# Kernel tuning notes

Measured on AMD Instinct MI355X. Metric: run time of the kernel, lower is better.

Reference implementation:

```python
import jax, jax.numpy as jnp
import numpy as np

G = 8
NEIGHBORS = 9
BN_EPS = 1e-5


def grid_sample_border(feat, grid):
    """Bilinear grid_sample, padding_mode='border', align_corners=False.
    feat: [B,C,H,W], grid: [B,Ho,Wo,2] in [-1,1] -> [B,C,Ho,Wo]."""
    B, C, H, W = feat.shape
    Ho, Wo = grid.shape[1], grid.shape[2]
    gx, gy = grid[..., 0], grid[..., 1]
    ix = jnp.clip(((gx + 1.0) * W - 1.0) * 0.5, 0.0, W - 1.0)
    iy = jnp.clip(((gy + 1.0) * H - 1.0) * 0.5, 0.0, H - 1.0)
    x0 = jnp.floor(ix)
    y0 = jnp.floor(iy)
    wx = (ix - x0).reshape(B, 1, Ho * Wo)
    wy = (iy - y0).reshape(B, 1, Ho * Wo)
    x0i = jnp.clip(x0.astype(jnp.int32), 0, W - 1)
    x1i = jnp.clip(x0i + 1, 0, W - 1)
    y0i = jnp.clip(y0.astype(jnp.int32), 0, H - 1)
    y1i = jnp.clip(y0i + 1, 0, H - 1)
    featf = feat.reshape(B, C, H * W)

    def gather(yi, xi):
        idx = (yi * W + xi).reshape(B, 1, Ho * Wo)
        return jnp.take_along_axis(featf, idx, axis=2)  # [B,C,Ho*Wo]

    v00 = gather(y0i, x0i)
    v01 = gather(y0i, x1i)
    v10 = gather(y1i, x0i)
    v11 = gather(y1i, x1i)
    out = (v00 * (1 - wx) * (1 - wy) + v01 * wx * (1 - wy)
           + v10 * (1 - wx) * wy + v11 * wx * wy)
    return out.reshape(B, C, Ho, Wo)


def bn3d(x, g, b, m, v):
    # inference-mode BatchNorm3d over channel axis 1 of [B,C,N,H,W]
    sh = (1, -1, 1, 1, 1)
    return g.reshape(sh) * (x - m.reshape(sh)) * jax.lax.rsqrt(v.reshape(sh) + BN_EPS) + b.reshape(sh)


def setup_inputs() -> dict:
    key = jax.random.key(0)
    ks = jax.random.split(key, 16)
    B, C, H, W = 2, 64, 256, 320
    ref_feature = jax.random.normal(ks[0], (B, C, H, W), dtype=jnp.float32)
    grid = jax.random.uniform(ks[1], (B, NEIGHBORS * H, W, 2), dtype=jnp.float32, minval=-1.0, maxval=1.0)
    p = lambda k, sh: 0.1 * jax.random.normal(k, sh, dtype=jnp.float32)
    return {
        "ref_feature": ref_feature,
        "grid": grid,
        "conv0_w": p(ks[2], (16, G)),
        "bn0_g": jnp.ones((16,), jnp.float32),
        "bn0_b": jnp.zeros((16,), jnp.float32),
        "bn0_m": p(ks[3], (16,)),
        "bn0_v": jax.random.uniform(ks[4], (16,), jnp.float32, 0.5, 1.5),
        "conv1_w": p(ks[5], (8, 16)),
        "bn1_g": jnp.ones((8,), jnp.float32),
        "bn1_b": jnp.zeros((8,), jnp.float32),
        "bn1_m": p(ks[6], (8,)),
        "bn1_v": jax.random.uniform(ks[7], (8,), jnp.float32, 0.5, 1.5),
        "sim_w": p(ks[8], (1, 8)),
        "sim_b": jnp.zeros((1,), jnp.float32),
    }


def reference(ref_feature, grid, conv0_w, bn0_g, bn0_b, bn0_m, bn0_v,
              conv1_w, bn1_g, bn1_b, bn1_m, bn1_v, sim_w, sim_b):
    B, C, H, W = ref_feature.shape
    Cg = C // G
    x = grid_sample_border(ref_feature, grid)            # [B,C,NB*H,W]
    x = x.reshape(B, G, Cg, NEIGHBORS, H, W)
    ref = ref_feature.reshape(B, G, Cg, H, W)
    corr = jnp.mean(x * ref[:, :, :, None], axis=2)      # [B,G,NB,H,W]
    h = jax.nn.relu(bn3d(jnp.einsum('oc,bcnhw->bonhw', conv0_w, corr), bn0_g, bn0_b, bn0_m, bn0_v))
    h = jax.nn.relu(bn3d(jnp.einsum('oc,bcnhw->bonhw', conv1_w, h), bn1_g, bn1_b, bn1_m, bn1_v))
    s = jnp.einsum('oc,bcnhw->bonhw', sim_w, h) + sim_b.reshape(1, 1, 1, 1, 1)
    return jax.nn.sigmoid(s[:, 0])                        # [B,NB,H,W]
```

## Files before the change

kernel.cpp:

```cpp
#include <hip/hip_runtime.h>
#include <hip/hip_bf16.h>

#define BB  2
#define CC  64
#define HH  256
#define WW  320
#define NNB 9
#define PIX_PER_B (NNB * HH * WW)
#define HW (HH * WW)

typedef unsigned int uint;

#define FEATT_BYTES ((size_t)BB * HH * WW * 64 * sizeof(ushort))
#define NWTS 304

#define OW0 0
#define OB0 128
#define OW1 144
#define OB1 272
#define OSW 280
#define OSB 288

__global__ __launch_bounds__(64) void fw_fold(
    const float* __restrict__ conv0_w, const float* __restrict__ bn0_g,
    const float* __restrict__ bn0_b, const float* __restrict__ bn0_m,
    const float* __restrict__ bn0_v, const float* __restrict__ conv1_w,
    const float* __restrict__ bn1_g, const float* __restrict__ bn1_b,
    const float* __restrict__ bn1_m, const float* __restrict__ bn1_v,
    const float* __restrict__ sim_w, const float* __restrict__ sim_b,
    float* __restrict__ wts) {
  const int t = threadIdx.x;
  if (t < 16) {
    float a = bn0_g[t] * rsqrtf(bn0_v[t] + 1e-5f);
    wts[OB0 + t] = bn0_b[t] - bn0_m[t] * a;
#pragma unroll
    for (int g = 0; g < 8; ++g) wts[OW0 + t * 8 + g] = conv0_w[t * 8 + g] * a;
  } else if (t < 24) {
    int o = t - 16;
    float a = bn1_g[o] * rsqrtf(bn1_v[o] + 1e-5f);
    wts[OB1 + o] = bn1_b[o] - bn1_m[o] * a;
#pragma unroll
    for (int c = 0; c < 16; ++c) wts[OW1 + o * 16 + c] = conv1_w[o * 16 + c] * a;
  } else if (t < 32) {
    wts[OSW + t - 24] = sim_w[t - 24];
    if (t == 31) wts[OSB] = sim_b[0];
  }
}

__global__ __launch_bounds__(256) void fw_transpose(const float* __restrict__ feat,
                                                    ushort* __restrict__ featT) {
  __shared__ float tile[64][65];
  const int b = blockIdx.z, h = blockIdx.y, w0 = blockIdx.x * 64;
  const int tid = threadIdx.x;
#pragma unroll
  for (int it = 0; it < 16; ++it) {
    int idx = it * 256 + tid;
    int c = idx >> 6, w = idx & 63;
    tile[c][w] = feat[((b * CC + c) * HH + h) * WW + w0 + w];
  }
  __syncthreads();
#pragma unroll
  for (int it = 0; it < 16; ++it) {
    int idx = it * 256 + tid;
    int w = idx >> 6, c = idx & 63;
    __hip_bfloat16 v = __float2bfloat16(tile[c][w]);
    featT[((b * HH + h) * WW + w0 + w) * 64 + c] = *(ushort*)&v;
  }
}

__device__ __forceinline__ float blo(uint u) { return __uint_as_float(u << 16); }
__device__ __forceinline__ float bhi(uint u) { return __uint_as_float(u & 0xffff0000u); }

__global__ __launch_bounds__(256) void fw_main4(
    const ushort* __restrict__ featT, const float* __restrict__ grid,
    const float* __restrict__ wts, float* __restrict__ out) {
  const int blk = blockIdx.x;
  const int xcd = blk & 7;
  const int jb = blk >> 3;
  const int b = xcd >> 2;
  const int lblk = jb * 4 + (xcd & 3);

  const int tid = threadIdx.x;
  const int lane = tid & 63;
  const int wid = tid >> 6;
  const int team = lane >> 3;
  const int lj = lane & 7;
  const int wbase = lblk * 256 + wid * 64;

  const ushort* __restrict__ fbT = featT + (size_t)b * ((size_t)HW * 64);

  float wx, wy;
  int off00, offc;
  {
    const int pix = wbase + lane;
    const float2 g2 =
        *(const float2*)(grid + (size_t)2 * ((size_t)b * PIX_PER_B + pix));
    float ix = fminf(fmaxf(((g2.x + 1.0f) * (float)WW - 1.0f) * 0.5f, 0.0f),
                     (float)(WW - 1));
    float iy = fminf(fmaxf(((g2.y + 1.0f) * (float)HH - 1.0f) * 0.5f, 0.0f),
                     (float)(HH - 1));
    int x0 = min((int)floorf(ix), WW - 2);
    int y0 = min((int)floorf(iy), HH - 2);
    wx = ix - (float)x0;
    wy = iy - (float)y0;
    off00 = (y0 * WW + x0) * 64;
    offc = (pix % HW) * 64;
  }

  float pc[8];

#define PERM(S, PX, PY, PO, PQ)                                                \
  {                                                                            \
    int src = (S)*8 + team;                                                    \
    PX = __shfl(wx, src);                                                      \
    PY = __shfl(wy, src);                                                      \
    PO = __shfl(off00, src);                                                   \
    PQ = __shfl(offc, src);                                                    \
  }

#define LOADS(PO, PQ, L)                                                       \
  {                                                                            \
    const ushort* base = fbT + PO + lj * 8;                                    \
    L[0] = *(const uint4*)(base);                                     \
    L[1] = *(const uint4*)(base + 64);                                \
    L[2] = *(const uint4*)(base + WW * 64);                           \
    L[3] = *(const uint4*)(base + WW * 64 + 64);                      \
    L[4] = *(const uint4*)(fbT + PQ + lj * 8);                     \
  }

#define CORRS(S, PX, PY, L)                                                    \
  {                                                                            \
    float e00 = (1.0f - PX) * (1.0f - PY);                                     \
    float e01 = PX * (1.0f - PY);                                              \
    float e10 = (1.0f - PX) * PY;                                              \
    float e11 = PX * PY;                                                       \
    const uint* ua = (const uint*)&L[0];                                       \
    const uint* ub = (const uint*)&L[1];                                       \
    const uint* uc = (const uint*)&L[2];                                       \
    const uint* ud = (const uint*)&L[3];                                       \
    const uint* ur = (const uint*)&L[4];                                       \
    float acc = 0.0f;                                                          \
    _Pragma("unroll") for (int k = 0; k < 4; ++k) {                            \
      float s0 = e00 * blo(ua[k]) + e01 * blo(ub[k]) + e10 * blo(uc[k]) +      \
                 e11 * blo(ud[k]);                                             \
      acc += s0 * blo(ur[k]);                                                  \
      float s1 = e00 * bhi(ua[k]) + e01 * bhi(ub[k]) + e10 * bhi(uc[k]) +      \
                 e11 * bhi(ud[k]);                                             \
      acc += s1 * bhi(ur[k]);                                                  \
    }                                                                          \
    pc[S] = acc * 0.125f;                                                      \
  }

  float px0, py0, px1, py1, px2, py2, px3, py3;
  int po0, pq0, po1, pq1, po2, pq2, po3, pq3;
  uint4 L0[5], L1[5], L2[5], L3[5];

  PERM(0, px0, py0, po0, pq0) LOADS(po0, pq0, L0)
  PERM(1, px1, py1, po1, pq1) LOADS(po1, pq1, L1)
  PERM(2, px2, py2, po2, pq2) LOADS(po2, pq2, L2)
  PERM(3, px3, py3, po3, pq3) LOADS(po3, pq3, L3)
  __builtin_amdgcn_sched_barrier(0);

  CORRS(0, px0, py0, L0)
  PERM(4, px0, py0, po0, pq0) LOADS(po0, pq0, L0)
  __builtin_amdgcn_sched_barrier(0);
  CORRS(1, px1, py1, L1)
  PERM(5, px1, py1, po1, pq1) LOADS(po1, pq1, L1)
  __builtin_amdgcn_sched_barrier(0);
  CORRS(2, px2, py2, L2)
  PERM(6, px2, py2, po2, pq2) LOADS(po2, pq2, L2)
  __builtin_amdgcn_sched_barrier(0);
  CORRS(3, px3, py3, L3)
  PERM(7, px3, py3, po3, pq3) LOADS(po3, pq3, L3)
  __builtin_amdgcn_sched_barrier(0);
  CORRS(4, px0, py0, L0)
  CORRS(5, px1, py1, L1)
  CORRS(6, px2, py2, L2)
  CORRS(7, px3, py3, L3)

#undef PERM
#undef LOADS
#undef CORRS

#pragma unroll
  for (int m = 1; m < 8; m <<= 1) {
    float tmp[8];
#pragma unroll
    for (int s = 0; s < 8; ++s) tmp[s] = pc[s];
#pragma unroll
    for (int s = 0; s < 8; ++s) {
      float r = __shfl_xor(tmp[s ^ m], m);
      pc[s] = (((lj & m) != 0) == ((s & m) != 0)) ? tmp[s] : r;
    }
  }

  float h0v[16];
#pragma unroll
  for (int o = 0; o < 16; ++o) {
    float s = wts[OB0 + o];
#pragma unroll
    for (int g = 0; g < 8; ++g) s += wts[OW0 + o * 8 + g] * pc[g];
    h0v[o] = fmaxf(s, 0.0f);
  }
  float h1v[8];
#pragma unroll
  for (int o = 0; o < 8; ++o) {
    float s = wts[OB1 + o];
#pragma unroll
    for (int c = 0; c < 16; ++c) s += wts[OW1 + o * 16 + c] * h0v[c];
    h1v[o] = fmaxf(s, 0.0f);
  }
  float s = wts[OSB];
#pragma unroll
  for (int c = 0; c < 8; ++c) s += wts[OSW + c] * h1v[c];

  out[(size_t)b * PIX_PER_B + wbase + lj * 8 + team] =
      1.0f / (1.0f + __expf(-s));
}

__global__ __launch_bounds__(256) void fw_main_fallback(
    const float* __restrict__ feat, const float* __restrict__ grid,
    const float* __restrict__ conv0_w, const float* __restrict__ bn0_g,
    const float* __restrict__ bn0_b, const float* __restrict__ bn0_m,
    const float* __restrict__ bn0_v, const float* __restrict__ conv1_w,
    const float* __restrict__ bn1_g, const float* __restrict__ bn1_b,
    const float* __restrict__ bn1_m, const float* __restrict__ bn1_v,
    const float* __restrict__ sim_w, const float* __restrict__ sim_b,
    float* __restrict__ out) {
  __shared__ float sW0[16 * 8], sB0[16], sW1[8 * 16], sB1[8], sSW[8], sSB[1];
  {
    const int tt = threadIdx.x;
    if (tt < 16) {
      float a = bn0_g[tt] * rsqrtf(bn0_v[tt] + 1e-5f);
      sB0[tt] = bn0_b[tt] - bn0_m[tt] * a;
#pragma unroll
      for (int g = 0; g < 8; ++g) sW0[tt * 8 + g] = conv0_w[tt * 8 + g] * a;
    } else if (tt < 24) {
      int o = tt - 16;
      float a = bn1_g[o] * rsqrtf(bn1_v[o] + 1e-5f);
      sB1[o] = bn1_b[o] - bn1_m[o] * a;
#pragma unroll
      for (int c = 0; c < 16; ++c) sW1[o * 16 + c] = conv1_w[o * 16 + c] * a;
    } else if (tt < 32) {
      sSW[tt - 24] = sim_w[tt - 24];
      if (tt == 31) sSB[0] = sim_b[0];
    }
  }
  __syncthreads();

  const int t = blockIdx.x * 256 + threadIdx.x;
  const int w = t % WW;
  const int tmp = t / WW;
  const int h = tmp & (HH - 1);
  const int nb = tmp >> 8;
  const int n = nb % NNB;
  const int b = nb / NNB;

  const float2 g2 =
      *(const float2*)(grid + (size_t)2 * (((size_t)((b * NNB + n) * HH + h)) * WW + w));
  float ix = fminf(fmaxf(((g2.x + 1.0f) * (float)WW - 1.0f) * 0.5f, 0.0f), (float)(WW - 1));
  float iy = fminf(fmaxf(((g2.y + 1.0f) * (float)HH - 1.0f) * 0.5f, 0.0f), (float)(HH - 1));
  float x0f = floorf(ix), y0f = floorf(iy);
  float wx = ix - x0f, wy = iy - y0f;
  int x0 = (int)x0f, y0 = (int)y0f;
  int x1 = min(x0 + 1, WW - 1), y1 = min(y0 + 1, HH - 1);
  float w00 = (1.0f - wx) * (1.0f - wy), w01 = wx * (1.0f - wy);
  float w10 = (1.0f - wx) * wy, w11 = wx * wy;

  float corr[8];
  const float* fbp = feat + (size_t)b * (CC * HH * WW);
#pragma unroll
  for (int g = 0; g < 8; ++g) {
    float acc = 0.0f;
    for (int ch = 0; ch < 8; ++ch) {
      const float* fc = fbp + (size_t)(g * 8 + ch) * (HH * WW);
      float sv = w00 * fc[y0 * WW + x0] + w01 * fc[y0 * WW + x1] +
                 w10 * fc[y1 * WW + x0] + w11 * fc[y1 * WW + x1];
      acc += sv * fc[h * WW + w];
    }
    corr[g] = acc * 0.125f;
  }

  float h0v[16];
#pragma unroll
  for (int o = 0; o < 16; ++o) {
    float s = sB0[o];
#pragma unroll
    for (int g = 0; g < 8; ++g) s += sW0[o * 8 + g] * corr[g];
    h0v[o] = fmaxf(s, 0.0f);
  }
  float h1v[8];
#pragma unroll
  for (int o = 0; o < 8; ++o) {
    float s = sB1[o];
#pragma unroll
    for (int c = 0; c < 16; ++c) s += sW1[o * 16 + c] * h0v[c];
    h1v[o] = fmaxf(s, 0.0f);
  }
  float s = sSB[0];
#pragma unroll
  for (int c = 0; c < 8; ++c) s += sSW[c] * h1v[c];
  out[t] = 1.0f / (1.0f + __expf(-s));
}

extern "C" void kernel_launch(void* const* d_in, const int* in_sizes, int n_in,
                              void* d_out, int out_size, void* d_ws, size_t ws_size,
                              hipStream_t stream) {
  const float* ref_feature = (const float*)d_in[0];
  const float* grid    = (const float*)d_in[1];
  const float* conv0_w = (const float*)d_in[2];
  const float* bn0_g   = (const float*)d_in[3];
  const float* bn0_b   = (const float*)d_in[4];
  const float* bn0_m   = (const float*)d_in[5];
  const float* bn0_v   = (const float*)d_in[6];
  const float* conv1_w = (const float*)d_in[7];
  const float* bn1_g   = (const float*)d_in[8];
  const float* bn1_b   = (const float*)d_in[9];
  const float* bn1_m   = (const float*)d_in[10];
  const float* bn1_v   = (const float*)d_in[11];
  const float* sim_w   = (const float*)d_in[12];
  const float* sim_b   = (const float*)d_in[13];
  float* out = (float*)d_out;

  const size_t need = FEATT_BYTES + NWTS * sizeof(float);

  if (ws_size >= need) {
    ushort* featT = (ushort*)d_ws;
    float* wts = (float*)((char*)d_ws + FEATT_BYTES);
    fw_fold<<<1, 64, 0, stream>>>(conv0_w, bn0_g, bn0_b, bn0_m, bn0_v,
                                  conv1_w, bn1_g, bn1_b, bn1_m, bn1_v,
                                  sim_w, sim_b, wts);
    fw_transpose<<<dim3(WW / 64, HH, BB), 256, 0, stream>>>(ref_feature, featT);
    fw_main4<<<BB * PIX_PER_B / 256, 256, 0, stream>>>(featT, grid, wts, out);
  } else {
    fw_main_fallback<<<BB * PIX_PER_B / 256, 256, 0, stream>>>(ref_feature, grid,
        conv0_w, bn0_g, bn0_b, bn0_m, bn0_v,
        conv1_w, bn1_g, bn1_b, bn1_m, bn1_v, sim_w, sim_b, out);
  }
}
```

Before: 104.2 us.

## Reuse center feature loads across three neighbors per wave

```diff
diff --git a/kernel.cpp b/kernel.cpp
--- a/kernel.cpp
+++ b/kernel.cpp
@@ -71,7 +71,7 @@
 __device__ __forceinline__ float blo(uint u) { return __uint_as_float(u << 16); }
 __device__ __forceinline__ float bhi(uint u) { return __uint_as_float(u & 0xffff0000u); }
 
-__global__ __launch_bounds__(256) void fw_main4(
+__global__ __launch_bounds__(256) void fw_main5(
     const ushort* __restrict__ featT, const float* __restrict__ grid,
     const float* __restrict__ wts, float* __restrict__ out) {
   const int blk = blockIdx.x;
@@ -85,47 +85,36 @@
   const int wid = tid >> 6;
   const int team = lane >> 3;
   const int lj = lane & 7;
-  const int wbase = lblk * 256 + wid * 64;
+
+  const int task = lblk * 4 + wid;
+  const int trip = task / 1280;
+  const int hwg = task % 1280;
+  const int hwbase = hwg * 64;
 
   const ushort* __restrict__ fbT = featT + (size_t)b * ((size_t)HW * 64);
 
-  float wx, wy;
-  int off00, offc;
-  {
-    const int pix = wbase + lane;
-    const float2 g2 =
-        *(const float2*)(grid + (size_t)2 * ((size_t)b * PIX_PER_B + pix));
-    float ix = fminf(fmaxf(((g2.x + 1.0f) * (float)WW - 1.0f) * 0.5f, 0.0f),
-                     (float)(WW - 1));
-    float iy = fminf(fmaxf(((g2.y + 1.0f) * (float)HH - 1.0f) * 0.5f, 0.0f),
-                     (float)(HH - 1));
-    int x0 = min((int)floorf(ix), WW - 2);
-    int y0 = min((int)floorf(iy), HH - 2);
-    wx = ix - (float)x0;
-    wy = iy - (float)y0;
-    off00 = (y0 * WW + x0) * 64;
-    offc = (pix % HW) * 64;
-  }
+  uint4 ctr[8];
+#pragma unroll
+  for (int s = 0; s < 8; ++s)
+    ctr[s] = *(const uint4*)(fbT + (hwbase + s * 8 + team) * 64 + lj * 8);
 
   float pc[8];
 
-#define PERM(S, PX, PY, PO, PQ)                                                \
+#define PERM(S, PX, PY, PO)                                                    \
   {                                                                            \
     int src = (S)*8 + team;                                                    \
     PX = __shfl(wx, src);                                                      \
     PY = __shfl(wy, src);                                                      \
     PO = __shfl(off00, src);                                                   \
-    PQ = __shfl(offc, src);                                                    \
-  }
-
-#define LOADS(PO, PQ, L)                                                       \
+  }
+
+#define LOADS(PO, L)                                                           \
   {                                                                            \
     const ushort* base = fbT + PO + lj * 8;                                    \
     L[0] = *(const uint4*)(base);                                     \
     L[1] = *(const uint4*)(base + 64);                                \
     L[2] = *(const uint4*)(base + WW * 64);                           \
     L[3] = *(const uint4*)(base + WW * 64 + 64);                      \
-    L[4] = *(const uint4*)(fbT + PQ + lj * 8);                     \
   }
 
 #define CORRS(S, PX, PY, L)                                                    \
@@ -138,7 +127,7 @@
     const uint* ub = (const uint*)&L[1];                                       \
     const uint* uc = (const uint*)&L[2];                                       \
     const uint* ud = (const uint*)&L[3];                                       \
-    const uint* ur = (const uint*)&L[4];                                       \
+    const uint* ur = (const uint*)&ctr[S];                                     \
     float acc = 0.0f;                                                          \
     _Pragma("unroll") for (int k = 0; k < 4; ++k) {                            \
       float s0 = e00 * blo(ua[k]) + e01 * blo(ub[k]) + e10 * blo(uc[k]) +      \
@@ -151,71 +140,86 @@
     pc[S] = acc * 0.125f;                                                      \
   }
 
-  float px0, py0, px1, py1, px2, py2, px3, py3;
-  int po0, pq0, po1, pq1, po2, pq2, po3, pq3;
-  uint4 L0[5], L1[5], L2[5], L3[5];
-
-  PERM(0, px0, py0, po0, pq0) LOADS(po0, pq0, L0)
-  PERM(1, px1, py1, po1, pq1) LOADS(po1, pq1, L1)
-  PERM(2, px2, py2, po2, pq2) LOADS(po2, pq2, L2)
-  PERM(3, px3, py3, po3, pq3) LOADS(po3, pq3, L3)
-  __builtin_amdgcn_sched_barrier(0);
-
-  CORRS(0, px0, py0, L0)
-  PERM(4, px0, py0, po0, pq0) LOADS(po0, pq0, L0)
-  __builtin_amdgcn_sched_barrier(0);
-  CORRS(1, px1, py1, L1)
-  PERM(5, px1, py1, po1, pq1) LOADS(po1, pq1, L1)
-  __builtin_amdgcn_sched_barrier(0);
-  CORRS(2, px2, py2, L2)
-  PERM(6, px2, py2, po2, pq2) LOADS(po2, pq2, L2)
-  __builtin_amdgcn_sched_barrier(0);
-  CORRS(3, px3, py3, L3)
-  PERM(7, px3, py3, po3, pq3) LOADS(po3, pq3, L3)
-  __builtin_amdgcn_sched_barrier(0);
-  CORRS(4, px0, py0, L0)
-  CORRS(5, px1, py1, L1)
-  CORRS(6, px2, py2, L2)
-  CORRS(7, px3, py3, L3)
+  for (int r = 0; r < 3; ++r) {
+    const int n = trip * 3 + r;
+
+    float wx, wy;
+    int off00;
+    {
+      const int hw = hwbase + lane;
+      const float2 g2 = *(const float2*)(grid +
+          (size_t)2 * ((size_t)(b * NNB + n) * HW + hw));
+      float ix = fminf(fmaxf(((g2.x + 1.0f) * (float)WW - 1.0f) * 0.5f, 0.0f),
+                       (float)(WW - 1));
+      float iy = fminf(fmaxf(((g2.y + 1.0f) * (float)HH - 1.0f) * 0.5f, 0.0f),
+                       (float)(HH - 1));
+      int x0 = min((int)floorf(ix), WW - 2);
+      int y0 = min((int)floorf(iy), HH - 2);
+      wx = ix - (float)x0;
+      wy = iy - (float)y0;
+      off00 = (y0 * WW + x0) * 64;
+    }
+
+    float pxA, pyA, pxB, pyB;
+    int poA, poB;
+    uint4 LA[4], LB[4];
+
+    PERM(0, pxA, pyA, poA) LOADS(poA, LA)
+    PERM(1, pxB, pyB, poB) LOADS(poB, LB)
+    CORRS(0, pxA, pyA, LA)
+    PERM(2, pxA, pyA, poA) LOADS(poA, LA)
+    CORRS(1, pxB, pyB, LB)
+    PERM(3, pxB, pyB, poB) LOADS(poB, LB)
+    CORRS(2, pxA, pyA, LA)
+    PERM(4, pxA, pyA, poA) LOADS(poA, LA)
+    CORRS(3, pxB, pyB, LB)
+    PERM(5, pxB, pyB, poB) LOADS(poB, LB)
+    CORRS(4, pxA, pyA, LA)
+    PERM(6, pxA, pyA, poA) LOADS(poA, LA)
+    CORRS(5, pxB, pyB, LB)
+    PERM(7, pxB, pyB, poB) LOADS(poB, LB)
+    CORRS(6, pxA, pyA, LA)
+    CORRS(7, pxB, pyB, LB)
+
+#pragma unroll
+    for (int m = 1; m < 8; m <<= 1) {
+      float tmp[8];
+#pragma unroll
+      for (int s = 0; s < 8; ++s) tmp[s] = pc[s];
+#pragma unroll
+      for (int s = 0; s < 8; ++s) {
+        float rr = __shfl_xor(tmp[s ^ m], m);
+        pc[s] = (((lj & m) != 0) == ((s & m) != 0)) ? tmp[s] : rr;
+      }
+    }
+
+    float h0v[16];
+#pragma unroll
+    for (int o = 0; o < 16; ++o) {
+      float s = wts[OB0 + o];
+#pragma unroll
+      for (int g = 0; g < 8; ++g) s += wts[OW0 + o * 8 + g] * pc[g];
+      h0v[o] = fmaxf(s, 0.0f);
+    }
+    float h1v[8];
+#pragma unroll
+    for (int o = 0; o < 8; ++o) {
+      float s = wts[OB1 + o];
+#pragma unroll
+      for (int c = 0; c < 16; ++c) s += wts[OW1 + o * 16 + c] * h0v[c];
+      h1v[o] = fmaxf(s, 0.0f);
+    }
+    float s = wts[OSB];
+#pragma unroll
+    for (int c = 0; c < 8; ++c) s += wts[OSW + c] * h1v[c];
+
+    out[(size_t)b * PIX_PER_B + (size_t)n * HW + hwbase + lj * 8 + team] =
+        1.0f / (1.0f + __expf(-s));
+  }
 
 #undef PERM
 #undef LOADS
 #undef CORRS
-
-#pragma unroll
-  for (int m = 1; m < 8; m <<= 1) {
-    float tmp[8];
-#pragma unroll
-    for (int s = 0; s < 8; ++s) tmp[s] = pc[s];
-#pragma unroll
-    for (int s = 0; s < 8; ++s) {
-      float r = __shfl_xor(tmp[s ^ m], m);
-      pc[s] = (((lj & m) != 0) == ((s & m) != 0)) ? tmp[s] : r;
-    }
-  }
-
-  float h0v[16];
-#pragma unroll
-  for (int o = 0; o < 16; ++o) {
-    float s = wts[OB0 + o];
-#pragma unroll
-    for (int g = 0; g < 8; ++g) s += wts[OW0 + o * 8 + g] * pc[g];
-    h0v[o] = fmaxf(s, 0.0f);
-  }
-  float h1v[8];
-#pragma unroll
-  for (int o = 0; o < 8; ++o) {
-    float s = wts[OB1 + o];
-#pragma unroll
-    for (int c = 0; c < 16; ++c) s += wts[OW1 + o * 16 + c] * h0v[c];
-    h1v[o] = fmaxf(s, 0.0f);
-  }
-  float s = wts[OSB];
-#pragma unroll
-  for (int c = 0; c < 8; ++c) s += wts[OSW + c] * h1v[c];
-
-  out[(size_t)b * PIX_PER_B + wbase + lj * 8 + team] =
-      1.0f / (1.0f + __expf(-s));
 }
 
 __global__ __launch_bounds__(256) void fw_main_fallback(
@@ -331,7 +335,7 @@
                                   conv1_w, bn1_g, bn1_b, bn1_m, bn1_v,
                                   sim_w, sim_b, wts);
     fw_transpose<<<dim3(WW / 64, HH, BB), 256, 0, stream>>>(ref_feature, featT);
-    fw_main4<<<BB * PIX_PER_B / 256, 256, 0, stream>>>(featT, grid, wts, out);
+    fw_main5<<<1920, 256, 0, stream>>>(featT, grid, wts, out);
   } else {
     fw_main_fallback<<<BB * PIX_PER_B / 256, 256, 0, stream>>>(ref_feature, grid,
         conv0_w, bn0_g, bn0_b, bn0_m, bn0_v,
```

After: 106.3 us. +2.0%, slower.
